# Performance work log

Hardware: AMD Instinct MI355X
Metric: run time of the kernel (lower is better)

The kernel has to match this reference:

```python
import jax, jax.numpy as jnp
import numpy as np

B, M, GRID = 4, 8192, 32          # batches, points per batch, voxel grid side
N = B * M
K = 8                              # knn neighbors (includes self at dist 0)
C_IN, C_OUT, H = 8, 8, 128
KEYB = 64                          # hash base (coords shifted +1 stay in [0,33])
EPS = 1e-5


def setup_inputs() -> dict:
    rng = np.random.default_rng(0)
    # unique occupied voxels per batch (ME SparseTensor requires unique coords)
    cs = []
    for b in range(B):
        lin = rng.choice(GRID ** 3, size=M, replace=False)
        x, y, z = lin // (GRID * GRID), (lin // GRID) % GRID, lin % GRID
        cs.append(np.stack([np.full(M, b), x, y, z], axis=1))
    coords = jnp.asarray(np.concatenate(cs, axis=0).astype(np.int32))  # [N,4]

    key = jax.random.key(0)
    ks = jax.random.split(key, 4)
    feats = jax.random.normal(ks[0], (N, C_IN), jnp.float32)
    w1 = jax.random.normal(ks[1], ((K + 1) * C_IN, H), jnp.float32) * 0.05  # 1x1 conv
    g1 = jnp.ones((H,), jnp.float32)
    b1 = jnp.zeros((H,), jnp.float32)
    w3 = jax.random.normal(ks[2], (27, H, H), jnp.float32) * 0.02          # 3^3 sparse conv
    g2 = jnp.ones((H,), jnp.float32)
    b2 = jnp.zeros((H,), jnp.float32)
    w_out = jax.random.normal(ks[3], (H, 2 * C_OUT), jnp.float32) * 0.05   # 1x1 conv
    return dict(coords=coords, feats=feats, w1=w1, g1=g1, b1=b1,
                w3=w3, g2=g2, b2=b2, w_out=w_out)


def _knn_idx(coords):
    # per-batch brute-force kNN on xyz (batch column segments the search)
    xyz = coords[:, 1:].astype(jnp.float32).reshape(B, M, 3)
    d2 = jnp.sum((xyz[:, :, None, :] - xyz[:, None, :, :]) ** 2, -1)  # [B,M,M]
    _, idx = jax.lax.top_k(-d2, K)                                     # [B,M,K]
    return (idx + (jnp.arange(B) * M)[:, None, None]).reshape(N, K)


def _bn(x, g, b):
    mu = jnp.mean(x, axis=0)
    var = jnp.var(x, axis=0)
    return (x - mu) * jax.lax.rsqrt(var + EPS) * g + b


def reference(coords, feats, w1, g1, b1, w3, g2, b2, w_out):
    # --- kNN gather-and-build: [center || k neighbor feats] -> (k+1)*C_in ---
    nbr = _knn_idx(coords)                                        # [N,K] int
    combined = jnp.concatenate([feats[:, None, :], feats[nbr]], axis=1)
    combined = combined.reshape(N, (K + 1) * C_IN)
    # --- neighbor_processor: 1x1 conv + BN + ReLU ---
    h = jax.nn.relu(_bn(combined @ w1, g1, b1))                   # [N,H]
    # --- context_predictor conv k=3: gather inputs at coord+offset via hash ---
    c = coords[:, 1:] + 1                                         # shift so offsets stay >= 0
    keys = ((coords[:, 0] * KEYB + c[:, 0]) * KEYB + c[:, 1]) * KEYB + c[:, 2]
    order = jnp.argsort(keys)
    skeys = keys[order]
    offs = jnp.stack(jnp.meshgrid(*([jnp.arange(-1, 2)] * 3), indexing='ij'),
                     axis=-1).reshape(27, 3)                      # {-1,0,1}^3
    okey = (offs[:, 0] * KEYB + offs[:, 1]) * KEYB + offs[:, 2]   # [27]
    q = keys[None, :] + okey[:, None]                             # [27,N]
    pos = jnp.clip(jnp.searchsorted(skeys, q), 0, N - 1)
    valid = skeys[pos] == q                                       # [27,N]
    j = order[pos]                                                # [27,N]
    gathered = jnp.where(valid[..., None], h[j], 0.0)             # [27,N,H]
    h2 = jnp.einsum('onc,ocd->nd', gathered, w3)                  # [N,H]
    h2 = jax.nn.relu(_bn(h2, g2, b2))
    # --- final 1x1 conv -> mean/scale ---
    return h2 @ w_out                                             # [N, 2*C_OUT]
```

## Files before the change

### kernel.cpp

```cpp
#include <hip/hip_runtime.h>
#include <hip/hip_bf16.h>

#define B_   4
#define M_   8192
#define N_   32768
#define H_   128
#define EPS_ 1e-5f
#define TBL  1048576
#define GUARD 8192

typedef short short8 __attribute__((ext_vector_type(8)));
typedef float f32x4  __attribute__((ext_vector_type(4)));

__global__ __launch_bounds__(256) void prep_kernel(const int* __restrict__ coords,
                                                   int* __restrict__ table,
                                                   int* __restrict__ packed,
                                                   int* __restrict__ keyb,
                                                   float* __restrict__ gsum,
                                                   unsigned int* __restrict__ hbz) {
    int n = blockIdx.x * 256 + threadIdx.x;
    int b = coords[4*n+0], x = coords[4*n+1], y = coords[4*n+2], z = coords[4*n+3];
    packed[n] = (x << 10) | (y << 5) | z;
    int key = ((b*64 + x+1)*64 + y+1)*64 + (z+1);
    keyb[n] = key;
    table[key] = n;
    if (blockIdx.x == 0) gsum[threadIdx.x] = 0.f;
    if (blockIdx.x == 1 && threadIdx.x < 64) hbz[threadIdx.x] = 0u;
}

__global__ __launch_bounds__(256) void w3pack_kernel(const float* __restrict__ w3,
                                                     ushort* __restrict__ w3f) {
    int t = blockIdx.x * 256 + threadIdx.x;
    int lane = t & 63;
    int ct   = (t >> 6) & 7;
    int ks   = (t >> 9) & 3;
    int o    = t >> 11;
    int quad = lane >> 4, l15 = lane & 15;
    int n = ct*16 + l15;
    const float* src = w3 + o*16384;
    ushort out8[8];
#pragma unroll
    for (int j = 0; j < 8; ++j) {
        int c = ks*32 + quad*8 + j;
        float v = src[c*128 + n];
        __hip_bfloat16 bv = __float2bfloat16(v);
        ushort u; __builtin_memcpy(&u, &bv, 2);
        out8[j] = u;
    }
    *(uint4*)&w3f[t*8] = *(uint4*)out8;
}

__global__ __launch_bounds__(256) void knn_window_kernel(const int* __restrict__ table,
                                                         const int* __restrict__ keyb,
                                                         int* __restrict__ nbr,
                                                         int* __restrict__ flagcnt,
                                                         int* __restrict__ flaglist) {
    __shared__ int okey_sh[125], d2_sh[125];
    __shared__ int tops[256 * 8];
    int tid = threadIdx.x;
    if (tid < 125) {
        int dx = tid / 25 - 2, rr = tid % 25, dy = rr / 5 - 2, dz = rr % 5 - 2;
        okey_sh[tid] = dx * 4096 + dy * 64 + dz;
        d2_sh[tid]   = dx*dx + dy*dy + dz*dz;
    }
    __syncthreads();

    int q   = blockIdx.x * 64 + (tid >> 2);
    int sub = tid & 3;
    int kb  = keyb[q];

    int top[8];
#pragma unroll
    for (int k = 0; k < 8; ++k) top[k] = 0x7FFFFFFF;

    int base = sub * 32;
    int cnt  = (sub == 3) ? 29 : 32;
    for (int i = 0; i < cnt; ++i) {
        int idx = base + i;
        int j = table[kb + okey_sh[idx]];
        if (j >= 0) {
            int key = (d2_sh[idx] << 13) | (j & 8191);
            if (key < top[7]) {
#pragma unroll
                for (int k = 7; k >= 1; --k)
                    top[k] = (key < top[k]) ? max(key, top[k-1]) : top[k];
                top[0] = min(key, top[0]);
            }
        }
    }
#pragma unroll
    for (int k = 0; k < 8; ++k) tops[tid*8 + k] = top[k];
    __syncthreads();

    if (sub == 0) {
        const int* L = &tops[tid*8];
        int ia0 = 0, ia1 = 0, ia2 = 0, ia3 = 0;
        int res[8];
#pragma unroll
        for (int k = 0; k < 8; ++k) {
            int v0 = L[ia0], v1 = L[8 + ia1], v2 = L[16 + ia2], v3 = L[24 + ia3];
            int m01 = min(v0, v1), m23 = min(v2, v3);
            int m = min(m01, m23);
            res[k] = m;
            if (m == v0) ++ia0; else if (m == v1) ++ia1;
            else if (m == v2) ++ia2; else ++ia3;
        }
        int bb = q & ~(M_-1);
        if ((res[7] >> 13) <= 8) {
#pragma unroll
            for (int k = 0; k < 8; ++k) nbr[q*8 + k] = bb + (res[k] & 8191);
        } else {
            int pos = atomicAdd(flagcnt, 1);
            flaglist[pos] = q;
        }
    }
}

__global__ __launch_bounds__(256) void knn_bf_kernel(const int* __restrict__ packed,
                                                     const int* __restrict__ flagcnt,
                                                     const int* __restrict__ flaglist,
                                                     int* __restrict__ nbr) {
    __shared__ int tops[256 * 8];
    int tid = threadIdx.x;
    int cnt = *flagcnt;
    for (int f = blockIdx.x; f < cnt; f += gridDim.x) {
        int n = flaglist[f];
        int bb = n & ~(M_-1);
        int p = packed[n];
        int qx = (p >> 10) & 31, qy = (p >> 5) & 31, qz = p & 31;
        int top[8];
#pragma unroll
        for (int k = 0; k < 8; ++k) top[k] = 0x7FFFFFFF;
        for (int j = tid; j < M_; j += 256) {
            int c = packed[bb + j];
            int dx = qx - ((c >> 10) & 31);
            int dy = qy - ((c >> 5) & 31);
            int dz = qz - (c & 31);
            int d2 = dx*dx + dy*dy + dz*dz;
            int key = (d2 << 13) | j;
            if (key < top[7]) {
#pragma unroll
                for (int k = 7; k >= 1; --k)
                    top[k] = (key < top[k]) ? max(key, top[k-1]) : top[k];
                top[0] = min(key, top[0]);
            }
        }
#pragma unroll
        for (int k = 0; k < 8; ++k) tops[tid*8 + k] = top[k];
        __syncthreads();
        for (int stride = 128; stride >= 1; stride >>= 1) {
            if (tid < stride) {
                int* A  = &tops[tid*8];
                int* Bp = &tops[(tid+stride)*8];
                int r[8]; int ia = 0, ib = 0;
#pragma unroll
                for (int k = 0; k < 8; ++k) {
                    int a = A[ia], b2 = Bp[ib];
                    if (a <= b2) { r[k] = a; ++ia; } else { r[k] = b2; ++ib; }
                }
#pragma unroll
                for (int k = 0; k < 8; ++k) A[k] = r[k];
            }
            __syncthreads();
        }
        if (tid == 0) {
#pragma unroll
            for (int k = 0; k < 8; ++k) nbr[n*8 + k] = bb + (tops[k] & 8191);
        }
        __syncthreads();
    }
}

__global__ __launch_bounds__(256) void h1_kernel(const float* __restrict__ feats,
                                                 const int* __restrict__ nbr,
                                                 const float* __restrict__ w1,
                                                 float* __restrict__ hpre) {
    __shared__ float comb[16][72];
    int tid = threadIdx.x;
    int rowbase = blockIdx.x * 16;
    if (tid < 144) {
        int r = tid / 9, s = tid % 9;
        int grow = rowbase + r;
        int idx = (s == 0) ? grow : nbr[grow*8 + (s-1)];
        const float4* f = (const float4*)(feats + idx * 8);
        float4 a = f[0], b = f[1];
        float* dp = &comb[r][s*8];
        dp[0]=a.x; dp[1]=a.y; dp[2]=a.z; dp[3]=a.w;
        dp[4]=b.x; dp[5]=b.y; dp[6]=b.z; dp[7]=b.w;
    }
    __syncthreads();
    int c = tid & 127, rh = tid >> 7;
    float acc[8];
#pragma unroll
    for (int i = 0; i < 8; ++i) acc[i] = 0.f;
    for (int s = 0; s < 72; ++s) {
        float w = w1[s*128 + c];
#pragma unroll
        for (int i = 0; i < 8; ++i)
            acc[i] += comb[rh*8 + i][s] * w;
    }
#pragma unroll
    for (int i = 0; i < 8; ++i)
        hpre[(rowbase + rh*8 + i)*128 + c] = acc[i];
}

__global__ __launch_bounds__(256) void reduce_kernel(const float* __restrict__ src,
                                                     float* __restrict__ part) {
    __shared__ float ssum[256], ssq[256];
    int tid = threadIdx.x;
    int c = tid & 127, halfr = tid >> 7;
    int rowbase = blockIdx.x * 128 + halfr * 64;
    float s = 0.f, q = 0.f;
    for (int i = 0; i < 64; ++i) {
        float v = src[(rowbase + i)*128 + c];
        s += v; q += v*v;
    }
    ssum[tid] = s; ssq[tid] = q;
    __syncthreads();
    if (tid < 128) {
        part[blockIdx.x*256 + tid]       = ssum[tid] + ssum[tid+128];
        part[blockIdx.x*256 + 128 + tid] = ssq[tid]  + ssq[tid+128];
    }
}

__global__ __launch_bounds__(128) void stats_kernel(const float* __restrict__ part,
                                                    const float* __restrict__ g,
                                                    const float* __restrict__ bias,
                                                    float* __restrict__ scale,
                                                    float* __restrict__ shift) {
    int c = threadIdx.x;
    float s = 0.f, q = 0.f;
    for (int b = 0; b < 256; ++b) {
        s += part[b*256 + c];
        q += part[b*256 + 128 + c];
    }
    float mu  = s / (float)N_;
    float var = q / (float)N_ - mu*mu;
    float inv = rsqrtf(var + EPS_);
    float sc  = inv * g[c];
    scale[c] = sc;
    shift[c] = bias[c] - mu * sc;
}

__global__ __launch_bounds__(128) void stats2_kernel(const float* __restrict__ gsum,
                                                     const float* __restrict__ g,
                                                     const float* __restrict__ bias,
                                                     float* __restrict__ scale,
                                                     float* __restrict__ shift) {
    int c = threadIdx.x;
    float s = gsum[c], q = gsum[128 + c];
    float mu  = s / (float)N_;
    float var = q / (float)N_ - mu*mu;
    float inv = rsqrtf(var + EPS_);
    float sc  = inv * g[c];
    scale[c] = sc;
    shift[c] = bias[c] - mu * sc;
}

__global__ __launch_bounds__(256) void bnrelu_bf16_kernel(const float* __restrict__ x,
                                                          const float* __restrict__ scale,
                                                          const float* __restrict__ shift,
                                                          ushort* __restrict__ y) {
    int i = blockIdx.x * 256 + threadIdx.x;
    float4 v = ((const float4*)x)[i];
    int c = (i * 4) & 127;
    v.x = fmaxf(0.f, v.x*scale[c]   + shift[c]);
    v.y = fmaxf(0.f, v.y*scale[c+1] + shift[c+1]);
    v.z = fmaxf(0.f, v.z*scale[c+2] + shift[c+2]);
    v.w = fmaxf(0.f, v.w*scale[c+3] + shift[c+3]);
    ushort o[4];
#pragma unroll
    for (int k = 0; k < 4; ++k) {
        float f = (&v.x)[k];
        __hip_bfloat16 bv = __float2bfloat16(f);
        __builtin_memcpy(&o[k], &bv, 2);
    }
    ((ushort4*)y)[i] = make_ushort4(o[0], o[1], o[2], o[3]);
}

#define CONV3_LDS 163840
#define GLL(src, dst) __builtin_amdgcn_global_load_lds( \
    (const __attribute__((address_space(1))) unsigned int*)(src), \
    (__attribute__((address_space(3))) unsigned int*)(dst), 16, 0, 0)

__device__ __forceinline__ int okey_of(int o) {
    int dx = o/9 - 1, dy = (o/3)%3 - 1, dz = o%3 - 1;
    return dx*4096 + dy*64 + dz;
}

__global__ __launch_bounds__(512) void conv3_mfma_kernel(const ushort* __restrict__ hb,
                                                         const ushort* __restrict__ w3f,
                                                         const int* __restrict__ table,
                                                         const int* __restrict__ keyb,
                                                         float* __restrict__ h2,
                                                         float* __restrict__ gsum) {
    extern __shared__ char smem_raw[];
    int tid = threadIdx.x;
    int lane = tid & 63, wid = tid >> 6;
    int quad = lane >> 4, l15 = lane & 15;
    int bid = blockIdx.x;
    int swz = (bid & 7) * 32 + (bid >> 3);
    int rowbase = swz * 128;
    int wr = wid >> 1;
    int cb = (wid & 1) * 4;

    int r0 = tid >> 4;
    int swzoff = ((tid & 15) ^ (r0 & 15)) << 3;
    int kb0 = keyb[rowbase + r0];
    int kb1 = keyb[rowbase + r0 + 32];
    int kb2 = keyb[rowbase + r0 + 64];
    int kb3 = keyb[rowbase + r0 + 96];

    int ok0 = okey_of(0), ok1 = okey_of(1), ok2 = okey_of(2);
    int j00 = table[kb0+ok0], j01 = table[kb1+ok0], j02 = table[kb2+ok0], j03 = table[kb3+ok0];
    int j10 = table[kb0+ok1], j11 = table[kb1+ok1], j12 = table[kb2+ok1], j13 = table[kb3+ok1];
    int jc0 = table[kb0+ok2], jc1 = table[kb1+ok2], jc2 = table[kb2+ok2], jc3 = table[kb3+ok2];

    GLL(hb + j00*128 + swzoff, smem_raw + 0     + ((0*512+tid) << 4));
    GLL(hb + j01*128 + swzoff, smem_raw + 0     + ((1*512+tid) << 4));
    GLL(hb + j02*128 + swzoff, smem_raw + 0     + ((2*512+tid) << 4));
    GLL(hb + j03*128 + swzoff, smem_raw + 0     + ((3*512+tid) << 4));
#pragma unroll
    for (int i = 0; i < 4; ++i) {
        int flat = i*512 + tid;
        GLL(w3f + flat*8, smem_raw + 98304 + (flat << 4));
    }
    GLL(hb + j10*128 + swzoff, smem_raw + 32768 + ((0*512+tid) << 4));
    GLL(hb + j11*128 + swzoff, smem_raw + 32768 + ((1*512+tid) << 4));
    GLL(hb + j12*128 + swzoff, smem_raw + 32768 + ((2*512+tid) << 4));
    GLL(hb + j13*128 + swzoff, smem_raw + 32768 + ((3*512+tid) << 4));

    f32x4 acc[2][4];
#pragma unroll
    for (int i = 0; i < 2; ++i)
#pragma unroll
        for (int c = 0; c < 4; ++c)
            acc[i][c] = (f32x4){0.f, 0.f, 0.f, 0.f};

    int aRd = 0, aNx = 32768, aW = 65536;
    int bRd = 98304, bW = 131072;

#pragma unroll 1
    for (int o = 0; o < 27; ++o) {
        asm volatile("s_waitcnt vmcnt(4)" ::: "memory");
        __builtin_amdgcn_s_barrier();

        int on = (o+3 < 27) ? o+3 : 26;
        int okn = okey_of(on);
        int jn0 = table[kb0+okn], jn1 = table[kb1+okn], jn2 = table[kb2+okn], jn3 = table[kb3+okn];

        int ob = (o+1 < 27) ? o+1 : 26;
        const ushort* wsrc = w3f + (ob << 14);
#pragma unroll
        for (int i = 0; i < 4; ++i) {
            int flat = i*512 + tid;
            GLL(wsrc + flat*8, smem_raw + bW + (flat << 4));
        }
        GLL(hb + jc0*128 + swzoff, smem_raw + aW + ((0*512+tid) << 4));
        GLL(hb + jc1*128 + swzoff, smem_raw + aW + ((1*512+tid) << 4));
        GLL(hb + jc2*128 + swzoff, smem_raw + aW + ((2*512+tid) << 4));
        GLL(hb + jc3*128 + swzoff, smem_raw + aW + ((3*512+tid) << 4));

        const ushort* Ac = (const ushort*)(smem_raw + aRd);
        const ushort* Bc = (const ushort*)(smem_raw + bRd);
#pragma unroll
        for (int ks = 0; ks < 4; ++ks) {
            short8 af[2], bfr[4];
#pragma unroll
            for (int i = 0; i < 2; ++i) {
                int lr = wr*32 + i*16 + l15;
                int chunk = (ks*4 + quad) ^ l15;
                af[i] = *(const short8*)&Ac[lr*128 + chunk*8];
            }
#pragma unroll
            for (int c = 0; c < 4; ++c)
                bfr[c] = *(const short8*)&Bc[((ks*8 + cb + c)*64 + lane) << 3];
#pragma unroll
            for (int i = 0; i < 2; ++i)
#pragma unroll
                for (int c = 0; c < 4; ++c)
                    acc[i][c] = __builtin_amdgcn_mfma_f32_16x16x32_bf16(af[i], bfr[c], acc[i][c], 0, 0, 0);
        }

        jc0 = jn0; jc1 = jn1; jc2 = jn2; jc3 = jn3;
        int t = aRd; aRd = aNx; aNx = aW; aW = t;
        t = bRd; bRd = bW; bW = t;
    }

    __syncthreads();

    float s[4], q[4];
#pragma unroll
    for (int c = 0; c < 4; ++c) { s[c] = 0.f; q[c] = 0.f; }
#pragma unroll
    for (int i = 0; i < 2; ++i)
#pragma unroll
        for (int c = 0; c < 4; ++c)
#pragma unroll
            for (int r = 0; r < 4; ++r) {
                int row = rowbase + wr*32 + i*16 + quad*4 + r;
                int col = (cb + c)*16 + l15;
                float v = acc[i][c][r];
                h2[row*128 + col] = v;
                s[c] += v; q[c] += v*v;
            }
    float* red = (float*)smem_raw;
    if (tid < 256) red[tid] = 0.f;
    __syncthreads();
#pragma unroll
    for (int c = 0; c < 4; ++c) {
        int col = (cb + c)*16 + l15;
        atomicAdd(&red[col], s[c]);
        atomicAdd(&red[128 + col], q[c]);
    }
    __syncthreads();
    if (tid < 256) atomicAdd(&gsum[tid], red[tid]);
}

__global__ __launch_bounds__(256) void out_kernel(const float* __restrict__ h2,
                                                  const float* __restrict__ wout,
                                                  const float* __restrict__ scale,
                                                  const float* __restrict__ shift,
                                                  float* __restrict__ out) {
    __shared__ float sc[128], sh[128];
    int tid = threadIdx.x;
    if (tid < 128) { sc[tid] = scale[tid]; sh[tid] = shift[tid]; }
    __syncthreads();
    int r = tid >> 4, d = tid & 15;
    int row = blockIdx.x * 16 + r;
    float acc = 0.f;
    for (int c = 0; c < 128; ++c) {
        float hv = fmaxf(0.f, fmaf(h2[row*128 + c], sc[c], sh[c]));
        acc = fmaf(hv, wout[c*16 + d], acc);
    }
    out[row*16 + d] = acc;
}

extern "C" void kernel_launch(void* const* d_in, const int* in_sizes, int n_in,
                              void* d_out, int out_size, void* d_ws, size_t ws_size,
                              hipStream_t stream) {
    const int*   coords = (const int*)d_in[0];
    const float* feats  = (const float*)d_in[1];
    const float* w1     = (const float*)d_in[2];
    const float* g1     = (const float*)d_in[3];
    const float* b1     = (const float*)d_in[4];
    const float* w3     = (const float*)d_in[5];
    const float* g2     = (const float*)d_in[6];
    const float* b2     = (const float*)d_in[7];
    const float* wout   = (const float*)d_in[8];
    float* out = (float*)d_out;

    char* ws = (char*)d_ws;
    int*    table_base = (int*)(ws);
    int*    table   = table_base + GUARD;
    int*    packed  = (int*)(ws + (4352u<<10));
    int*    keyb    = (int*)(ws + (4608u<<10));
    int*    nbr     = (int*)(ws + (4864u<<10));
    int*    flagcnt = (int*)(ws + (5888u<<10));
    int*    flaglist= (int*)(ws + (5892u<<10));
    float*  part    = (float*)(ws + (6144u<<10));
    float*  scale1  = (float*)(ws + (6400u<<10));
    float*  shift1  = scale1 + 128;
    float*  scale2  = shift1 + 128;
    float*  shift2  = scale2 + 128;
    float*  gsum    = (float*)(ws + (6416u<<10));
    ushort* w3f     = (ushort*)(ws + (6656u<<10));
    ushort* hb      = (ushort*)(ws + (7680u<<10));
    float*  h       = (float*)(ws + (15872u<<10));
    float*  h2      = h;

    static bool conv3_attr_set = false;
    if (!conv3_attr_set) {
        hipFuncSetAttribute(reinterpret_cast<const void*>(&conv3_mfma_kernel),
                            hipFuncAttributeMaxDynamicSharedMemorySize, CONV3_LDS);
        conv3_attr_set = true;
    }

    hipMemsetAsync(table_base, 0xFF, (TBL + GUARD) * sizeof(int), stream);
    hipMemsetAsync(flagcnt, 0, sizeof(int), stream);
    prep_kernel      <<<N_/256, 256, 0, stream>>>(coords, table, packed, keyb,
                                                  gsum, (unsigned int*)(hb - 128));
    w3pack_kernel    <<<216, 256, 0, stream>>>(w3, w3f);
    knn_window_kernel<<<N_/64, 256, 0, stream>>>(table, keyb, nbr, flagcnt, flaglist);
    knn_bf_kernel    <<<256, 256, 0, stream>>>(packed, flagcnt, flaglist, nbr);
    h1_kernel        <<<N_/16, 256, 0, stream>>>(feats, nbr, w1, h);
    reduce_kernel    <<<N_/128, 256, 0, stream>>>(h, part);
    stats_kernel     <<<1, 128, 0, stream>>>(part, g1, b1, scale1, shift1);
    bnrelu_bf16_kernel<<<(N_*H_/4)/256, 256, 0, stream>>>(h, scale1, shift1, hb);
    conv3_mfma_kernel<<<N_/128, 512, CONV3_LDS, stream>>>(hb, w3f, table, keyb, h2, gsum);
    stats2_kernel    <<<1, 128, 0, stream>>>(gsum, g2, b2, scale2, shift2);
    out_kernel       <<<N_/16, 256, 0, stream>>>(h2, wout, scale2, shift2, out);
}
```

Before: 227.3 us.

## Load conv3 gathered rows into registers and tile out_kernel through LDS

```diff
diff --git a/kernel.cpp b/kernel.cpp
--- a/kernel.cpp
+++ b/kernel.cpp
@@ -278,7 +278,7 @@
     ((ushort4*)y)[i] = make_ushort4(o[0], o[1], o[2], o[3]);
 }
 
-#define CONV3_LDS 163840
+#define CONV3_LDS 79872
 #define GLL(src, dst) __builtin_amdgcn_global_load_lds( \
     (const __attribute__((address_space(1))) unsigned int*)(src), \
     (__attribute__((address_space(3))) unsigned int*)(dst), 16, 0, 0)
@@ -295,6 +295,7 @@
                                                          float* __restrict__ h2,
                                                          float* __restrict__ gsum) {
     extern __shared__ char smem_raw[];
+    int* jsh = (int*)(smem_raw + 65536);
     int tid = threadIdx.x;
     int lane = tid & 63, wid = tid >> 6;
     int quad = lane >> 4, l15 = lane & 15;
@@ -304,31 +305,31 @@
     int wr = wid >> 1;
     int cb = (wid & 1) * 4;
 
-    int r0 = tid >> 4;
-    int swzoff = ((tid & 15) ^ (r0 & 15)) << 3;
-    int kb0 = keyb[rowbase + r0];
-    int kb1 = keyb[rowbase + r0 + 32];
-    int kb2 = keyb[rowbase + r0 + 64];
-    int kb3 = keyb[rowbase + r0 + 96];
-
-    int ok0 = okey_of(0), ok1 = okey_of(1), ok2 = okey_of(2);
-    int j00 = table[kb0+ok0], j01 = table[kb1+ok0], j02 = table[kb2+ok0], j03 = table[kb3+ok0];
-    int j10 = table[kb0+ok1], j11 = table[kb1+ok1], j12 = table[kb2+ok1], j13 = table[kb3+ok1];
-    int jc0 = table[kb0+ok2], jc1 = table[kb1+ok2], jc2 = table[kb2+ok2], jc3 = table[kb3+ok2];
-
-    GLL(hb + j00*128 + swzoff, smem_raw + 0     + ((0*512+tid) << 4));
-    GLL(hb + j01*128 + swzoff, smem_raw + 0     + ((1*512+tid) << 4));
-    GLL(hb + j02*128 + swzoff, smem_raw + 0     + ((2*512+tid) << 4));
-    GLL(hb + j03*128 + swzoff, smem_raw + 0     + ((3*512+tid) << 4));
+    for (int t = tid; t < 27*128; t += 512) {
+        int o = t >> 7, r = t & 127;
+        jsh[t] = table[keyb[rowbase + r] + okey_of(o)];
+    }
+    __syncthreads();
+
+    int row0 = wr*32 + l15;
+    int row1 = row0 + 16;
+
+    short8 aC[8], aN[8];
+    {
+        int j0 = jsh[row0], j1 = jsh[row1];
+        const ushort* p0 = hb + j0*128 + quad*8;
+        const ushort* p1 = hb + j1*128 + quad*8;
+#pragma unroll
+        for (int ks = 0; ks < 4; ++ks) {
+            aC[ks*2+0] = *(const short8*)(p0 + ks*32);
+            aC[ks*2+1] = *(const short8*)(p1 + ks*32);
+        }
+    }
 #pragma unroll
     for (int i = 0; i < 4; ++i) {
         int flat = i*512 + tid;
-        GLL(w3f + flat*8, smem_raw + 98304 + (flat << 4));
-    }
-    GLL(hb + j10*128 + swzoff, smem_raw + 32768 + ((0*512+tid) << 4));
-    GLL(hb + j11*128 + swzoff, smem_raw + 32768 + ((1*512+tid) << 4));
-    GLL(hb + j12*128 + swzoff, smem_raw + 32768 + ((2*512+tid) << 4));
-    GLL(hb + j13*128 + swzoff, smem_raw + 32768 + ((3*512+tid) << 4));
+        GLL(w3f + flat*8, smem_raw + (flat << 4));
+    }
 
     f32x4 acc[2][4];
 #pragma unroll
@@ -337,54 +338,46 @@
         for (int c = 0; c < 4; ++c)
             acc[i][c] = (f32x4){0.f, 0.f, 0.f, 0.f};
 
-    int aRd = 0, aNx = 32768, aW = 65536;
-    int bRd = 98304, bW = 131072;
-
 #pragma unroll 1
     for (int o = 0; o < 27; ++o) {
-        asm volatile("s_waitcnt vmcnt(4)" ::: "memory");
+        asm volatile("s_waitcnt vmcnt(0)" ::: "memory");
         __builtin_amdgcn_s_barrier();
-
-        int on = (o+3 < 27) ? o+3 : 26;
-        int okn = okey_of(on);
-        int jn0 = table[kb0+okn], jn1 = table[kb1+okn], jn2 = table[kb2+okn], jn3 = table[kb3+okn];
-
-        int ob = (o+1 < 27) ? o+1 : 26;
-        const ushort* wsrc = w3f + (ob << 14);
-#pragma unroll
-        for (int i = 0; i < 4; ++i) {
-            int flat = i*512 + tid;
-            GLL(wsrc + flat*8, smem_raw + bW + (flat << 4));
-        }
-        GLL(hb + jc0*128 + swzoff, smem_raw + aW + ((0*512+tid) << 4));
-        GLL(hb + jc1*128 + swzoff, smem_raw + aW + ((1*512+tid) << 4));
-        GLL(hb + jc2*128 + swzoff, smem_raw + aW + ((2*512+tid) << 4));
-        GLL(hb + jc3*128 + swzoff, smem_raw + aW + ((3*512+tid) << 4));
-
-        const ushort* Ac = (const ushort*)(smem_raw + aRd);
-        const ushort* Bc = (const ushort*)(smem_raw + bRd);
+        __builtin_amdgcn_sched_barrier(0);
+        int on = (o+1 < 27) ? o+1 : 26;
+        {
+            int jn0 = jsh[on*128 + row0], jn1 = jsh[on*128 + row1];
+            const ushort* p0 = hb + jn0*128 + quad*8;
+            const ushort* p1 = hb + jn1*128 + quad*8;
+#pragma unroll
+            for (int ks = 0; ks < 4; ++ks) {
+                aN[ks*2+0] = *(const short8*)(p0 + ks*32);
+                aN[ks*2+1] = *(const short8*)(p1 + ks*32);
+            }
+        }
+        {
+            const ushort* wsrc = w3f + (on << 14);
+            char* bdst = smem_raw + (((o+1) & 1) << 15);
+#pragma unroll
+            for (int i = 0; i < 4; ++i) {
+                int flat = i*512 + tid;
+                GLL(wsrc + flat*8, bdst + (flat << 4));
+            }
+        }
+        const ushort* Bc = (const ushort*)(smem_raw + ((o & 1) << 15));
 #pragma unroll
         for (int ks = 0; ks < 4; ++ks) {
-            short8 af[2], bfr[4];
-#pragma unroll
-            for (int i = 0; i < 2; ++i) {
-                int lr = wr*32 + i*16 + l15;
-                int chunk = (ks*4 + quad) ^ l15;
-                af[i] = *(const short8*)&Ac[lr*128 + chunk*8];
-            }
+            short8 bfr[4];
 #pragma unroll
             for (int c = 0; c < 4; ++c)
                 bfr[c] = *(const short8*)&Bc[((ks*8 + cb + c)*64 + lane) << 3];
 #pragma unroll
-            for (int i = 0; i < 2; ++i)
-#pragma unroll
-                for (int c = 0; c < 4; ++c)
-                    acc[i][c] = __builtin_amdgcn_mfma_f32_16x16x32_bf16(af[i], bfr[c], acc[i][c], 0, 0, 0);
-        }
-
-        jc0 = jn0; jc1 = jn1; jc2 = jn2; jc3 = jn3;
-        int t = aRd; aRd = aNx; aNx = aW; aW = t;
-        t = bRd; bRd = bW; bW = t;
+            for (int c = 0; c < 4; ++c) {
+                acc[0][c] = __builtin_amdgcn_mfma_f32_16x16x32_bf16(aC[ks*2+0], bfr[c], acc[0][c], 0, 0, 0);
+                acc[1][c] = __builtin_amdgcn_mfma_f32_16x16x32_bf16(aC[ks*2+1], bfr[c], acc[1][c], 0, 0, 0);
+            }
+        }
+#pragma unroll
+        for (int k = 0; k < 8; ++k) aC[k] = aN[k];
     }
 
     __syncthreads();
@@ -422,18 +415,50 @@
                                                   const float* __restrict__ scale,
                                                   const float* __restrict__ shift,
                                                   float* __restrict__ out) {
+    __shared__ float hrow[128][129];
+    __shared__ float wsh[2048];
     __shared__ float sc[128], sh[128];
     int tid = threadIdx.x;
     if (tid < 128) { sc[tid] = scale[tid]; sh[tid] = shift[tid]; }
-    __syncthreads();
-    int r = tid >> 4, d = tid & 15;
-    int row = blockIdx.x * 16 + r;
-    float acc = 0.f;
+#pragma unroll
+    for (int i = 0; i < 8; ++i) wsh[i*256 + tid] = wout[i*256 + tid];
+    __syncthreads();
+
+    int rowbase = blockIdx.x * 128;
+#pragma unroll
+    for (int i = 0; i < 16; ++i) {
+        int flat = i*256 + tid;
+        int row = flat >> 5, c4 = (flat & 31) * 4;
+        float4 v = *(const float4*)&h2[(rowbase + row)*128 + c4];
+        float4 scv = *(const float4*)&sc[c4];
+        float4 shv = *(const float4*)&sh[c4];
+        hrow[row][c4+0] = fmaxf(0.f, fmaf(v.x, scv.x, shv.x));
+        hrow[row][c4+1] = fmaxf(0.f, fmaf(v.y, scv.y, shv.y));
+        hrow[row][c4+2] = fmaxf(0.f, fmaf(v.z, scv.z, shv.z));
+        hrow[row][c4+3] = fmaxf(0.f, fmaf(v.w, scv.w, shv.w));
+    }
+    __syncthreads();
+
+    int row = tid >> 1, dbase = (tid & 1) * 8;
+    float acc[8];
+#pragma unroll
+    for (int k = 0; k < 8; ++k) acc[k] = 0.f;
     for (int c = 0; c < 128; ++c) {
-        float hv = fmaxf(0.f, fmaf(h2[row*128 + c], sc[c], sh[c]));
-        acc = fmaf(hv, wout[c*16 + d], acc);
-    }
-    out[row*16 + d] = acc;
+        float hv = hrow[row][c];
+        float4 w0 = *(const float4*)&wsh[c*16 + dbase];
+        float4 w1 = *(const float4*)&wsh[c*16 + dbase + 4];
+        acc[0] = fmaf(hv, w0.x, acc[0]);
+        acc[1] = fmaf(hv, w0.y, acc[1]);
+        acc[2] = fmaf(hv, w0.z, acc[2]);
+        acc[3] = fmaf(hv, w0.w, acc[3]);
+        acc[4] = fmaf(hv, w1.x, acc[4]);
+        acc[5] = fmaf(hv, w1.y, acc[5]);
+        acc[6] = fmaf(hv, w1.z, acc[6]);
+        acc[7] = fmaf(hv, w1.w, acc[7]);
+    }
+    float* op = out + (rowbase + row)*16 + dbase;
+    *(float4*)op       = (float4){acc[0], acc[1], acc[2], acc[3]};
+    *(float4*)(op + 4) = (float4){acc[4], acc[5], acc[6], acc[7]};
 }
 
 extern "C" void kernel_launch(void* const* d_in, const int* in_sizes, int n_in,
@@ -489,5 +514,5 @@
     bnrelu_bf16_kernel<<<(N_*H_/4)/256, 256, 0, stream>>>(h, scale1, shift1, hb);
     conv3_mfma_kernel<<<N_/128, 512, CONV3_LDS, stream>>>(hb, w3f, table, keyb, h2, gsum);
     stats2_kernel    <<<1, 128, 0, stream>>>(gsum, g2, b2, scale2, shift2);
-    out_kernel       <<<N_/16, 256, 0, stream>>>(h2, wout, scale2, shift2, out);
-}
+    out_kernel       <<<N_/128, 256, 0, stream>>>(h2, wout, scale2, shift2, out);
+}
```

Result: slower. 235.6 us (+3.7%).
